# Kernel tuning notes

Hardware: AMD Instinct MI355X
Metric: run time of the kernel (lower is better)

## Reference

```python
import jax, jax.numpy as jnp
import numpy as np

SCALE = 8.0  # sqrt(d_head=64), per init_kwargs
B, H, S, D = 2, 16, 2048, 64


def setup_inputs() -> dict:
    key = jax.random.key(0)
    kq, kk, kv = jax.random.split(key, 3)
    q = jax.random.normal(kq, (B, H, S, D), dtype=jnp.float32)
    k = jax.random.normal(kk, (B, H, S, D), dtype=jnp.float32)
    v = jax.random.normal(kv, (B, H, S, D), dtype=jnp.float32)
    # causal mask: True where attention is NOT allowed (strictly upper triangle)
    causal = jnp.triu(jnp.ones((S, S), dtype=bool), k=1)
    mask = jnp.broadcast_to(causal, (B, H, S, S))
    return {"q": q, "k": k, "v": v, "mask": mask}


def reference(q, k, v, mask):
    # score = (q @ k^T) / scale, masked_fill(mask, -inf), softmax, @ v
    score = jnp.einsum('bhqd,bhkd->bhqk', q, k) / SCALE
    score = jnp.where(mask, -jnp.inf, score)
    attn = jax.nn.softmax(score, axis=-1)
    output = jnp.einsum('bhqk,bhkd->bhqd', attn, v)
    return (attn, output)
```

## Files before the change

kernel.cpp:

```cpp
#include <hip/hip_runtime.h>
#include <hip/hip_bf16.h>

#define S_LEN 2048
#define D_HEAD 64
#define SD (S_LEN * D_HEAD)
#define TILE_B 8192
#define NTILES 32

typedef __attribute__((ext_vector_type(8))) short short8;
typedef __attribute__((ext_vector_type(4))) float f32x4;

__device__ __forceinline__ unsigned short f2b(float f) {
  unsigned int u = __float_as_uint(f);
  u += 0x7fffu + ((u >> 16) & 1u);
  return (unsigned short)(u >> 16);
}

__device__ __forceinline__ float b2f(unsigned short s) {
  return __uint_as_float(((unsigned int)s) << 16);
}

__device__ __forceinline__ void gl_lds16(const void* g, void* l) {
  __builtin_amdgcn_global_load_lds(
      (const __attribute__((address_space(1))) unsigned int*)g,
      (__attribute__((address_space(3))) unsigned int*)l, 16, 0, 0);
}

__device__ __forceinline__ void stage8k(const char* gsrc, char* ldst, int w, int lane) {
  gl_lds16(gsrc + ((w * 64 + lane) << 4),        ldst + ((w * 64) << 4));
  gl_lds16(gsrc + ((256 + w * 64 + lane) << 4),  ldst + ((256 + w * 64) << 4));
}

__global__ __launch_bounds__(256) void convert_kv_kernel(
    const float* __restrict__ K, const float* __restrict__ V,
    char* __restrict__ Kpre, char* __restrict__ Vpre) {
  const int bid = blockIdx.x;
  const int tid = threadIdx.x;
  if (bid < 1024) {
    const int bh = bid >> 5, tile = bid & 31;
    const float* Kb = K + (size_t)bh * SD + tile * 64 * 64;
    char* out = Kpre + (size_t)bid * TILE_B;
    #pragma unroll
    for (int j = 0; j < 2; ++j) {
      int c = tid + j * 256;
      int sl = c >> 3;
      int d0 = ((c & 7) ^ (sl & 7)) << 3;
      const float* src = Kb + sl * 64 + d0;
      float4 a = *(const float4*)src;
      float4 b = *(const float4*)(src + 4);
      short8 o;
      o[0]=(short)f2b(a.x); o[1]=(short)f2b(a.y); o[2]=(short)f2b(a.z); o[3]=(short)f2b(a.w);
      o[4]=(short)f2b(b.x); o[5]=(short)f2b(b.y); o[6]=(short)f2b(b.z); o[7]=(short)f2b(b.w);
      *(short8*)(out + c * 16) = o;
    }
  } else {
    __shared__ float Vl[64][65];
    const int vb = bid - 1024;
    const int bh = vb >> 5, tile = vb & 31;
    const float* Vb = V + (size_t)bh * SD + tile * 64 * 64;
    #pragma unroll
    for (int j = 0; j < 4; ++j) {
      int row = (tid >> 4) + j * 16;
      int c4 = (tid & 15) << 2;
      float4 v = *(const float4*)(Vb + row * 64 + c4);
      Vl[row][c4+0] = v.x; Vl[row][c4+1] = v.y; Vl[row][c4+2] = v.z; Vl[row][c4+3] = v.w;
    }
    __syncthreads();
    char* out = Vpre + (size_t)vb * TILE_B;
    #pragma unroll
    for (int j = 0; j < 2; ++j) {
      int c = tid + j * 256;
      int d = c >> 3;
      int s0 = ((c & 7) ^ ((d >> 2) & 7)) << 3;
      short8 o;
      #pragma unroll
      for (int i = 0; i < 8; ++i) o[i] = (short)f2b(Vl[s0 + i][d]);
      *(short8*)(out + c * 16) = o;
    }
  }
}

__global__ __launch_bounds__(256, 4) void sdpa_pre_kernel(
    const float* __restrict__ Qg, const char* __restrict__ Kpre,
    const char* __restrict__ Vpre, float* __restrict__ attn,
    float* __restrict__ outp) {
  const int j  = blockIdx.x >> 8;
  const int rr = blockIdx.x & 255;
  const int xcd = rr & 7;
  const int cu  = rr >> 3;
  const int bh  = xcd + ((cu & 3) << 3);
  const int u   = cu >> 2;
  const int qt  = (j == 0) ? u : (j == 1) ? (15 - u) : (j == 2) ? (16 + u) : (31 - u);

  const int tid = threadIdx.x, wave = tid >> 6, lane = tid & 63;
  const int g = lane >> 4, m = lane & 15;
  const int swzK = (m & 7) << 4;

  __shared__ __align__(16) unsigned short Kl[2][4096];
  __shared__ __align__(16) unsigned short Vt[2][4096];
  __shared__ __align__(16) unsigned short Pl[4][1024];
  char* const PB = (char*)(&Pl[wave][0]);

  const size_t bhSD = (size_t)bh * SD;
  const size_t bhSS = (size_t)bh << 22;
  const char* KpreBH = Kpre + (size_t)bh * NTILES * TILE_B;
  const char* VpreBH = Vpre + (size_t)bh * NTILES * TILE_B;

  int vro[4], vsz[4];
  #pragma unroll
  for (int dc = 0; dc < 4; ++dc) {
    int d = dc * 16 + m;
    vro[dc] = d << 7;
    vsz[dc] = ((d >> 2) & 7) << 4;
  }
  const float SCL = 0.18033688011112042f;

  const int q0 = qt << 6;
  const int nIt = qt + 1;
  const int qwrow = q0 + wave * 16;
  const int qbase = qwrow + g * 4;

  short8 aq0, aq1;
  {
    const float* qp = Qg + bhSD + (size_t)(qwrow + m) * D_HEAD + g * 8;
    float4 x0 = *(const float4*)(qp);
    float4 x1 = *(const float4*)(qp + 4);
    float4 y0 = *(const float4*)(qp + 32);
    float4 y1 = *(const float4*)(qp + 36);
    aq0[0]=(short)f2b(x0.x*SCL); aq0[1]=(short)f2b(x0.y*SCL);
    aq0[2]=(short)f2b(x0.z*SCL); aq0[3]=(short)f2b(x0.w*SCL);
    aq0[4]=(short)f2b(x1.x*SCL); aq0[5]=(short)f2b(x1.y*SCL);
    aq0[6]=(short)f2b(x1.z*SCL); aq0[7]=(short)f2b(x1.w*SCL);
    aq1[0]=(short)f2b(y0.x*SCL); aq1[1]=(short)f2b(y0.y*SCL);
    aq1[2]=(short)f2b(y0.z*SCL); aq1[3]=(short)f2b(y0.w*SCL);
    aq1[4]=(short)f2b(y1.x*SCL); aq1[5]=(short)f2b(y1.y*SCL);
    aq1[6]=(short)f2b(y1.z*SCL); aq1[7]=(short)f2b(y1.w*SCL);
  }

  float rs0 = 0.f, rs1 = 0.f, rs2 = 0.f, rs3 = 0.f;
  __builtin_amdgcn_s_barrier();
  stage8k(KpreBH, (char*)Kl[0], wave, lane);
  int cur = 0;
  for (int it = 0; it < nIt; ++it) {
    asm volatile("s_waitcnt vmcnt(0)" ::: "memory");
    __builtin_amdgcn_s_barrier();
    __builtin_amdgcn_sched_barrier(0);
    if (it + 1 < nIt)
      stage8k(KpreBH + (size_t)(it + 1) * TILE_B, (char*)Kl[cur ^ 1], wave, lane);
    asm volatile("" ::: "memory");
    const char* KB = (const char*)Kl[cur];
    const int kc = it << 6;
    #pragma unroll
    for (int t = 0; t < 4; ++t) {
      f32x4 acc = {0.f, 0.f, 0.f, 0.f};
      const int rb = (t * 16 + m) << 7;
      short8 b0 = *(const short8*)(KB + ((rb + g * 16) ^ swzK));
      short8 b1 = *(const short8*)(KB + ((rb + 64 + g * 16) ^ swzK));
      acc = __builtin_amdgcn_mfma_f32_16x16x32_bf16(aq0, b0, acc, 0, 0, 0);
      acc = __builtin_amdgcn_mfma_f32_16x16x32_bf16(aq1, b1, acc, 0, 0, 0);
      const int kcol = kc + t * 16 + m;
      rs0 += (kcol <= qbase + 0) ? exp2f(acc[0]) : 0.f;
      rs1 += (kcol <= qbase + 1) ? exp2f(acc[1]) : 0.f;
      rs2 += (kcol <= qbase + 2) ? exp2f(acc[2]) : 0.f;
      rs3 += (kcol <= qbase + 3) ? exp2f(acc[3]) : 0.f;
    }
    cur ^= 1;
  }
  #pragma unroll
  for (int sft = 1; sft < 16; sft <<= 1) {
    rs0 += __shfl_xor(rs0, sft, 64);
    rs1 += __shfl_xor(rs1, sft, 64);
    rs2 += __shfl_xor(rs2, sft, 64);
    rs3 += __shfl_xor(rs3, sft, 64);
  }
  const float ri0 = 1.f / rs0, ri1 = 1.f / rs1, ri2 = 1.f / rs2, ri3 = 1.f / rs3;

  f32x4 o0 = {0.f,0.f,0.f,0.f}, o1 = {0.f,0.f,0.f,0.f};
  f32x4 o2 = {0.f,0.f,0.f,0.f}, o3 = {0.f,0.f,0.f,0.f};
  __builtin_amdgcn_s_barrier();
  stage8k(KpreBH, (char*)Kl[0], wave, lane);
  stage8k(VpreBH, (char*)Vt[0], wave, lane);
  cur = 0;
  const int sr = lane >> 2;
  const int cq = lane & 3;
  for (int it = 0; it < nIt; ++it) {
    if (it == 0) { asm volatile("s_waitcnt vmcnt(0)" ::: "memory"); }
    else         { asm volatile("s_waitcnt vmcnt(4)" ::: "memory"); }
    __builtin_amdgcn_s_barrier();
    __builtin_amdgcn_sched_barrier(0);
    if (it + 1 < nIt) {
      stage8k(KpreBH + (size_t)(it + 1) * TILE_B, (char*)Kl[cur ^ 1], wave, lane);
      stage8k(VpreBH + (size_t)(it + 1) * TILE_B, (char*)Vt[cur ^ 1], wave, lane);
    }
    asm volatile("" ::: "memory");
    const char* KB = (const char*)Kl[cur];
    const char* VB = (const char*)Vt[cur];
    const int kc = it << 6;
    #pragma unroll
    for (int t = 0; t < 4; ++t) {
      f32x4 acc = {0.f, 0.f, 0.f, 0.f};
      const int rb = (t * 16 + m) << 7;
      short8 b0 = *(const short8*)(KB + ((rb + g * 16) ^ swzK));
      short8 b1 = *(const short8*)(KB + ((rb + 64 + g * 16) ^ swzK));
      acc = __builtin_amdgcn_mfma_f32_16x16x32_bf16(aq0, b0, acc, 0, 0, 0);
      acc = __builtin_amdgcn_mfma_f32_16x16x32_bf16(aq1, b1, acc, 0, 0, 0);
      const int kcol = kc + t * 16 + m;
      const int tc = t * 16 + m;
      float p0 = (kcol <= qbase + 0) ? exp2f(acc[0]) * ri0 : 0.f;
      float p1 = (kcol <= qbase + 1) ? exp2f(acc[1]) * ri1 : 0.f;
      float p2 = (kcol <= qbase + 2) ? exp2f(acc[2]) * ri2 : 0.f;
      float p3 = (kcol <= qbase + 3) ? exp2f(acc[3]) * ri3 : 0.f;
      const int r0 = g * 4, c2 = tc << 1;
      *(unsigned short*)(PB + ((((r0+0)<<7) + c2) ^ (((r0+0)&7)<<4))) = f2b(p0);
      *(unsigned short*)(PB + ((((r0+1)<<7) + c2) ^ (((r0+1)&7)<<4))) = f2b(p1);
      *(unsigned short*)(PB + ((((r0+2)<<7) + c2) ^ (((r0+2)&7)<<4))) = f2b(p2);
      *(unsigned short*)(PB + ((((r0+3)<<7) + c2) ^ (((r0+3)&7)<<4))) = f2b(p3);
    }
    {
      float* arow = attn + bhSS + (size_t)(qwrow + sr) * S_LEN + kc + cq * 16;
      #pragma unroll
      for (int h = 0; h < 2; ++h) {
        const int off = (((sr << 7) + (cq << 5) + (h << 4))) ^ ((sr & 7) << 4);
        short8 pr = *(const short8*)(PB + off);
        float4 fa, fb;
        fa.x = b2f((unsigned short)pr[0]); fa.y = b2f((unsigned short)pr[1]);
        fa.z = b2f((unsigned short)pr[2]); fa.w = b2f((unsigned short)pr[3]);
        fb.x = b2f((unsigned short)pr[4]); fb.y = b2f((unsigned short)pr[5]);
        fb.z = b2f((unsigned short)pr[6]); fb.w = b2f((unsigned short)pr[7]);
        *(float4*)(arow + 8 * h)     = fa;
        *(float4*)(arow + 8 * h + 4) = fb;
      }
    }
    short8 pa0 = *(const short8*)(PB + (((m << 7) + g * 16) ^ swzK));
    short8 pa1 = *(const short8*)(PB + (((m << 7) + 64 + g * 16) ^ swzK));
    #pragma unroll
    for (int dc = 0; dc < 4; ++dc) {
      short8 bv0 = *(const short8*)(VB + ((vro[dc] + g * 16) ^ vsz[dc]));
      short8 bv1 = *(const short8*)(VB + ((vro[dc] + 64 + g * 16) ^ vsz[dc]));
      f32x4& od = (dc == 0) ? o0 : (dc == 1) ? o1 : (dc == 2) ? o2 : o3;
      od = __builtin_amdgcn_mfma_f32_16x16x32_bf16(pa0, bv0, od, 0, 0, 0);
      od = __builtin_amdgcn_mfma_f32_16x16x32_bf16(pa1, bv1, od, 0, 0, 0);
    }
    cur ^= 1;
  }

  #pragma unroll
  for (int reg = 0; reg < 4; ++reg) {
    float* op = outp + bhSD + (size_t)(qbase + reg) * D_HEAD + m;
    op[ 0] = o0[reg];
    op[16] = o1[reg];
    op[32] = o2[reg];
    op[48] = o3[reg];
  }

  const int col0 = nIt << 6;
  const int nvec = (S_LEN - col0) >> 2;
  if (nvec > 0) {
    const float4 z = {0.f, 0.f, 0.f, 0.f};
    for (int r = 0; r < 64; ++r) {
      float4* rp = (float4*)(attn + bhSS + (size_t)(q0 + r) * S_LEN + col0);
      for (int i = tid; i < nvec; i += 256) rp[i] = z;
    }
  }
}

__global__ __launch_bounds__(256) void sdpa_fb_kernel(
    const float* __restrict__ Qg, const float* __restrict__ Kg,
    const float* __restrict__ Vg, float* __restrict__ attn,
    float* __restrict__ outp) {
  const int bh = blockIdx.x >> 4;
  const int pi = blockIdx.x & 15;
  const int tid  = threadIdx.x;
  const int wave = tid >> 6;
  const int lane = tid & 63;
  const int g = lane >> 4;
  const int m = lane & 15;
  const int swzK = (m & 7) << 4;
  __shared__ __align__(16) unsigned short Kl[2][64 * 64];
  __shared__ __align__(16) unsigned short Vt[2][64 * 64];
  __shared__ __align__(16) unsigned short Pl[4][16 * 64];
  char* const PB = (char*)(&Pl[wave][0]);
  const size_t bhSD = (size_t)bh * (S_LEN * D_HEAD);
  const size_t bhSS = (size_t)bh * ((size_t)S_LEN * S_LEN);
  int ss[4], dd[4], koff[4];
  #pragma unroll
  for (int j = 0; j < 4; ++j) {
    int f = tid + j * 256;
    ss[j] = f >> 4;
    dd[j] = (f & 15) << 2;
    koff[j] = (((ss[j] << 6) + dd[j]) << 1) ^ ((ss[j] & 7) << 4);
  }
  int vro[4], vsz[4];
  #pragma unroll
  for (int dc = 0; dc < 4; ++dc) {
    int d = dc * 16 + m;
    vro[dc] = d << 7;
    vsz[dc] = ((d >> 2) & 7) << 4;
  }
  const float SCL = 0.18033688011112042f;
  for (int sidx = 0; sidx < 2; ++sidx) {
    const int qt = sidx ? (31 - pi) : pi;
    const int q0 = qt << 6;
    const int kmax = q0 + 64;
    const int nIter = kmax >> 6;
    const int qwrow = q0 + wave * 16;
    const int qbase = qwrow + g * 4;
    short8 aq0, aq1;
    {
      const float* qp = Qg + bhSD + (size_t)(qwrow + m) * D_HEAD + g * 8;
      float4 x0 = *(const float4*)(qp);
      float4 x1 = *(const float4*)(qp + 4);
      float4 y0 = *(const float4*)(qp + 32);
      float4 y1 = *(const float4*)(qp + 36);
      aq0[0]=(short)f2b(x0.x*SCL); aq0[1]=(short)f2b(x0.y*SCL);
      aq0[2]=(short)f2b(x0.z*SCL); aq0[3]=(short)f2b(x0.w*SCL);
      aq0[4]=(short)f2b(x1.x*SCL); aq0[5]=(short)f2b(x1.y*SCL);
      aq0[6]=(short)f2b(x1.z*SCL); aq0[7]=(short)f2b(x1.w*SCL);
      aq1[0]=(short)f2b(y0.x*SCL); aq1[1]=(short)f2b(y0.y*SCL);
      aq1[2]=(short)f2b(y0.z*SCL); aq1[3]=(short)f2b(y0.w*SCL);
      aq1[4]=(short)f2b(y1.x*SCL); aq1[5]=(short)f2b(y1.y*SCL);
      aq1[6]=(short)f2b(y1.z*SCL); aq1[7]=(short)f2b(y1.w*SCL);
    }
    float rs0 = 0.f, rs1 = 0.f, rs2 = 0.f, rs3 = 0.f;
    {
      float4 kr[4];
      #pragma unroll
      for (int j = 0; j < 4; ++j)
        kr[j] = *(const float4*)(Kg + bhSD + (size_t)ss[j] * D_HEAD + dd[j]);
      #pragma unroll
      for (int j = 0; j < 4; ++j) {
        ushort4 kb;
        kb.x = f2b(kr[j].x); kb.y = f2b(kr[j].y);
        kb.z = f2b(kr[j].z); kb.w = f2b(kr[j].w);
        *(ushort4*)((char*)Kl[0] + koff[j]) = kb;
      }
    }
    __syncthreads();
    int cur = 0;
    for (int it = 0; it < nIter; ++it) {
      const int kc = it << 6;
      const bool pf = (it + 1 < nIter);
      float4 kr[4];
      if (pf) {
        #pragma unroll
        for (int j = 0; j < 4; ++j)
          kr[j] = *(const float4*)(Kg + bhSD + (size_t)(kc + 64 + ss[j]) * D_HEAD + dd[j]);
      }
      const char* KB = (const char*)Kl[cur];
      #pragma unroll
      for (int t = 0; t < 4; ++t) {
        f32x4 acc = {0.f, 0.f, 0.f, 0.f};
        const int rb = (t * 16 + m) << 7;
        short8 b0 = *(const short8*)(KB + ((rb + g * 16) ^ swzK));
        short8 b1 = *(const short8*)(KB + ((rb + 64 + g * 16) ^ swzK));
        acc = __builtin_amdgcn_mfma_f32_16x16x32_bf16(aq0, b0, acc, 0, 0, 0);
        acc = __builtin_amdgcn_mfma_f32_16x16x32_bf16(aq1, b1, acc, 0, 0, 0);
        const int kcol = kc + t * 16 + m;
        rs0 += (kcol <= qbase + 0) ? exp2f(acc[0]) : 0.f;
        rs1 += (kcol <= qbase + 1) ? exp2f(acc[1]) : 0.f;
        rs2 += (kcol <= qbase + 2) ? exp2f(acc[2]) : 0.f;
        rs3 += (kcol <= qbase + 3) ? exp2f(acc[3]) : 0.f;
      }
      if (pf) {
        #pragma unroll
        for (int j = 0; j < 4; ++j) {
          ushort4 kb;
          kb.x = f2b(kr[j].x); kb.y = f2b(kr[j].y);
          kb.z = f2b(kr[j].z); kb.w = f2b(kr[j].w);
          *(ushort4*)((char*)Kl[cur ^ 1] + koff[j]) = kb;
        }
      }
      __syncthreads();
      cur ^= 1;
    }
    #pragma unroll
    for (int sft = 1; sft < 16; sft <<= 1) {
      rs0 += __shfl_xor(rs0, sft, 64);
      rs1 += __shfl_xor(rs1, sft, 64);
      rs2 += __shfl_xor(rs2, sft, 64);
      rs3 += __shfl_xor(rs3, sft, 64);
    }
    const float ri0 = 1.f / rs0, ri1 = 1.f / rs1, ri2 = 1.f / rs2, ri3 = 1.f / rs3;
    f32x4 o0 = {0.f,0.f,0.f,0.f}, o1 = {0.f,0.f,0.f,0.f};
    f32x4 o2 = {0.f,0.f,0.f,0.f}, o3 = {0.f,0.f,0.f,0.f};
    {
      float4 kr[4], vr[4];
      #pragma unroll
      for (int j = 0; j < 4; ++j) {
        kr[j] = *(const float4*)(Kg + bhSD + (size_t)ss[j] * D_HEAD + dd[j]);
        vr[j] = *(const float4*)(Vg + bhSD + (size_t)ss[j] * D_HEAD + dd[j]);
      }
      #pragma unroll
      for (int j = 0; j < 4; ++j) {
        ushort4 kb;
        kb.x = f2b(kr[j].x); kb.y = f2b(kr[j].y);
        kb.z = f2b(kr[j].z); kb.w = f2b(kr[j].w);
        *(ushort4*)((char*)Kl[0] + koff[j]) = kb;
        const int d0 = dd[j], s2 = ss[j] << 1;
        char* VB1 = (char*)Vt[0];
        *(unsigned short*)(VB1 + ((((d0+0)<<7) + s2) ^ ((((d0+0)>>2)&7)<<4))) = f2b(vr[j].x);
        *(unsigned short*)(VB1 + ((((d0+1)<<7) + s2) ^ ((((d0+1)>>2)&7)<<4))) = f2b(vr[j].y);
        *(unsigned short*)(VB1 + ((((d0+2)<<7) + s2) ^ ((((d0+2)>>2)&7)<<4))) = f2b(vr[j].z);
        *(unsigned short*)(VB1 + ((((d0+3)<<7) + s2) ^ ((((d0+3)>>2)&7)<<4))) = f2b(vr[j].w);
      }
    }
    __syncthreads();
    cur = 0;
    for (int it = 0; it < nIter; ++it) {
      const int kc = it << 6;
      const bool pf = (it + 1 < nIter);
      float4 kr[4], vr[4];
      if (pf) {
        #pragma unroll
        for (int j = 0; j < 4; ++j) {
          kr[j] = *(const float4*)(Kg + bhSD + (size_t)(kc + 64 + ss[j]) * D_HEAD + dd[j]);
          vr[j] = *(const float4*)(Vg + bhSD + (size_t)(kc + 64 + ss[j]) * D_HEAD + dd[j]);
        }
      }
      const char* KB = (const char*)Kl[cur];
      const char* VB = (const char*)Vt[cur];
      float* arow = attn + bhSS + (size_t)qbase * S_LEN + kc;
      #pragma unroll
      for (int t = 0; t < 4; ++t) {
        f32x4 acc = {0.f, 0.f, 0.f, 0.f};
        const int rb = (t * 16 + m) << 7;
        short8 b0 = *(const short8*)(KB + ((rb + g * 16) ^ swzK));
        short8 b1 = *(const short8*)(KB + ((rb + 64 + g * 16) ^ swzK));
        acc = __builtin_amdgcn_mfma_f32_16x16x32_bf16(aq0, b0, acc, 0, 0, 0);
        acc = __builtin_amdgcn_mfma_f32_16x16x32_bf16(aq1, b1, acc, 0, 0, 0);
        const int kcol = kc + t * 16 + m;
        const int tc = t * 16 + m;
        float p0 = (kcol <= qbase + 0) ? exp2f(acc[0]) * ri0 : 0.f;
        float p1 = (kcol <= qbase + 1) ? exp2f(acc[1]) * ri1 : 0.f;
        float p2 = (kcol <= qbase + 2) ? exp2f(acc[2]) * ri2 : 0.f;
        float p3 = (kcol <= qbase + 3) ? exp2f(acc[3]) * ri3 : 0.f;
        arow[0 * S_LEN + tc] = p0;
        arow[1 * S_LEN + tc] = p1;
        arow[2 * S_LEN + tc] = p2;
        arow[3 * S_LEN + tc] = p3;
        const int r0 = g * 4, c2 = tc << 1;
        *(unsigned short*)(PB + ((((r0+0)<<7) + c2) ^ (((r0+0)&7)<<4))) = f2b(p0);
        *(unsigned short*)(PB + ((((r0+1)<<7) + c2) ^ (((r0+1)&7)<<4))) = f2b(p1);
        *(unsigned short*)(PB + ((((r0+2)<<7) + c2) ^ (((r0+2)&7)<<4))) = f2b(p2);
        *(unsigned short*)(PB + ((((r0+3)<<7) + c2) ^ (((r0+3)&7)<<4))) = f2b(p3);
      }
      short8 pa0 = *(const short8*)(PB + (((m << 7) + g * 16) ^ swzK));
      short8 pa1 = *(const short8*)(PB + (((m << 7) + 64 + g * 16) ^ swzK));
      #pragma unroll
      for (int dc = 0; dc < 4; ++dc) {
        short8 bv0 = *(const short8*)(VB + ((vro[dc] + g * 16) ^ vsz[dc]));
        short8 bv1 = *(const short8*)(VB + ((vro[dc] + 64 + g * 16) ^ vsz[dc]));
        f32x4& od = (dc == 0) ? o0 : (dc == 1) ? o1 : (dc == 2) ? o2 : o3;
        od = __builtin_amdgcn_mfma_f32_16x16x32_bf16(pa0, bv0, od, 0, 0, 0);
        od = __builtin_amdgcn_mfma_f32_16x16x32_bf16(pa1, bv1, od, 0, 0, 0);
      }
      if (pf) {
        #pragma unroll
        for (int j = 0; j < 4; ++j) {
          ushort4 kb;
          kb.x = f2b(kr[j].x); kb.y = f2b(kr[j].y);
          kb.z = f2b(kr[j].z); kb.w = f2b(kr[j].w);
          *(ushort4*)((char*)Kl[cur ^ 1] + koff[j]) = kb;
          const int d0 = dd[j], s2 = ss[j] << 1;
          char* VB1 = (char*)Vt[cur ^ 1];
          *(unsigned short*)(VB1 + ((((d0+0)<<7) + s2) ^ ((((d0+0)>>2)&7)<<4))) = f2b(vr[j].x);
          *(unsigned short*)(VB1 + ((((d0+1)<<7) + s2) ^ ((((d0+1)>>2)&7)<<4))) = f2b(vr[j].y);
          *(unsigned short*)(VB1 + ((((d0+2)<<7) + s2) ^ ((((d0+2)>>2)&7)<<4))) = f2b(vr[j].z);
          *(unsigned short*)(VB1 + ((((d0+3)<<7) + s2) ^ ((((d0+3)>>2)&7)<<4))) = f2b(vr[j].w);
        }
      }
      __syncthreads();
      cur ^= 1;
    }
    #pragma unroll
    for (int reg = 0; reg < 4; ++reg) {
      float* op = outp + bhSD + (size_t)(qbase + reg) * D_HEAD + m;
      op[ 0] = o0[reg];
      op[16] = o1[reg];
      op[32] = o2[reg];
      op[48] = o3[reg];
    }
    const int ncols = S_LEN - kmax;
    if (ncols > 0) {
      const float4 z = {0.f, 0.f, 0.f, 0.f};
      const int nvec = ncols >> 2;
      for (int r = 0; r < 64; ++r) {
        float4* rp = (float4*)(attn + bhSS + (size_t)(q0 + r) * S_LEN + kmax);
        for (int i = tid; i < nvec; i += 256) rp[i] = z;
      }
    }
  }
}

extern "C" void kernel_launch(void* const* d_in, const int* in_sizes, int n_in,
                              void* d_out, int out_size, void* d_ws, size_t ws_size,
                              hipStream_t stream) {
  (void)in_sizes; (void)n_in; (void)out_size;
  const float* q = (const float*)d_in[0];
  const float* k = (const float*)d_in[1];
  const float* v = (const float*)d_in[2];
  float* attn = (float*)d_out;
  float* outp = attn + (size_t)2 * 16 * 2048 * 2048;
  const size_t pre_bytes = (size_t)32 * NTILES * TILE_B;
  if (ws_size >= 2 * pre_bytes) {
    char* Kpre = (char*)d_ws;
    char* Vpre = Kpre + pre_bytes;
    convert_kv_kernel<<<2048, 256, 0, stream>>>(k, v, Kpre, Vpre);
    sdpa_pre_kernel<<<1024, 256, 0, stream>>>(q, Kpre, Vpre, attn, outp);
  } else {
    sdpa_fb_kernel<<<512, 256, 0, stream>>>(q, k, v, attn, outp);
  }
}
```

Baseline: 179.8 us.

## Interleave attention zero-fill into first pass and specialize unmasked tiles

Moves the zero-filling of the masked upper-triangle attn region out of the kernel tail and spreads it across the iterations of the first (row-sum) pass. The global stores can then overlap with the MFMA and exp work instead of running as a serial epilogue. It also splits both passes into a fast path for tiles fully below the diagonal, which skips the per-element causal compare, and keeps the masked path for diagonal tiles. The cost is larger code and added integer division work in the fill loop. The fill's stores may also compete with the K staging loads.

```diff
diff --git a/kernel.cpp b/kernel.cpp
--- a/kernel.cpp
+++ b/kernel.cpp
@@ -137,6 +137,14 @@
     aq1[6]=(short)f2b(y1.z*SCL); aq1[7]=(short)f2b(y1.w*SCL);
   }
 
+  const int ncols = S_LEN - (nIt << 6);
+  const int nvpr = ncols >> 2;
+  const int T = ncols >> 4;
+  const int F = (T + nIt - 1) / nIt;
+  int vb = 0;
+  float* const fillb = attn + bhSS + (size_t)q0 * S_LEN + (nIt << 6);
+  const float4 z4 = {0.f, 0.f, 0.f, 0.f};
+
   float rs0 = 0.f, rs1 = 0.f, rs2 = 0.f, rs3 = 0.f;
   __builtin_amdgcn_s_barrier();
   stage8k(KpreBH, (char*)Kl[0], wave, lane);
@@ -147,22 +155,47 @@
     __builtin_amdgcn_sched_barrier(0);
     if (it + 1 < nIt)
       stage8k(KpreBH + (size_t)(it + 1) * TILE_B, (char*)Kl[cur ^ 1], wave, lane);
+    if (T > 0) {
+      int ve = vb + F; if (ve > T) ve = T;
+      for (; vb < ve; ++vb) {
+        int gv = vb * 256 + tid;
+        int row = (unsigned)gv / (unsigned)nvpr;
+        int cv = gv - row * nvpr;
+        *(float4*)(fillb + (size_t)row * S_LEN + (cv << 2)) = z4;
+      }
+    }
     asm volatile("" ::: "memory");
     const char* KB = (const char*)Kl[cur];
     const int kc = it << 6;
-    #pragma unroll
-    for (int t = 0; t < 4; ++t) {
-      f32x4 acc = {0.f, 0.f, 0.f, 0.f};
-      const int rb = (t * 16 + m) << 7;
-      short8 b0 = *(const short8*)(KB + ((rb + g * 16) ^ swzK));
-      short8 b1 = *(const short8*)(KB + ((rb + 64 + g * 16) ^ swzK));
-      acc = __builtin_amdgcn_mfma_f32_16x16x32_bf16(aq0, b0, acc, 0, 0, 0);
-      acc = __builtin_amdgcn_mfma_f32_16x16x32_bf16(aq1, b1, acc, 0, 0, 0);
-      const int kcol = kc + t * 16 + m;
-      rs0 += (kcol <= qbase + 0) ? exp2f(acc[0]) : 0.f;
-      rs1 += (kcol <= qbase + 1) ? exp2f(acc[1]) : 0.f;
-      rs2 += (kcol <= qbase + 2) ? exp2f(acc[2]) : 0.f;
-      rs3 += (kcol <= qbase + 3) ? exp2f(acc[3]) : 0.f;
+    if (kc + 64 <= qwrow) {
+      #pragma unroll
+      for (int t = 0; t < 4; ++t) {
+        f32x4 acc = {0.f, 0.f, 0.f, 0.f};
+        const int rb = (t * 16 + m) << 7;
+        short8 b0 = *(const short8*)(KB + ((rb + g * 16) ^ swzK));
+        short8 b1 = *(const short8*)(KB + ((rb + 64 + g * 16) ^ swzK));
+        acc = __builtin_amdgcn_mfma_f32_16x16x32_bf16(aq0, b0, acc, 0, 0, 0);
+        acc = __builtin_amdgcn_mfma_f32_16x16x32_bf16(aq1, b1, acc, 0, 0, 0);
+        rs0 += exp2f(acc[0]);
+        rs1 += exp2f(acc[1]);
+        rs2 += exp2f(acc[2]);
+        rs3 += exp2f(acc[3]);
+      }
+    } else {
+      #pragma unroll
+      for (int t = 0; t < 4; ++t) {
+        f32x4 acc = {0.f, 0.f, 0.f, 0.f};
+        const int rb = (t * 16 + m) << 7;
+        short8 b0 = *(const short8*)(KB + ((rb + g * 16) ^ swzK));
+        short8 b1 = *(const short8*)(KB + ((rb + 64 + g * 16) ^ swzK));
+        acc = __builtin_amdgcn_mfma_f32_16x16x32_bf16(aq0, b0, acc, 0, 0, 0);
+        acc = __builtin_amdgcn_mfma_f32_16x16x32_bf16(aq1, b1, acc, 0, 0, 0);
+        const int kcol = kc + t * 16 + m;
+        rs0 += (kcol <= qbase + 0) ? exp2f(acc[0]) : 0.f;
+        rs1 += (kcol <= qbase + 1) ? exp2f(acc[1]) : 0.f;
+        rs2 += (kcol <= qbase + 2) ? exp2f(acc[2]) : 0.f;
+        rs3 += (kcol <= qbase + 3) ? exp2f(acc[3]) : 0.f;
+      }
     }
     cur ^= 1;
   }
@@ -196,25 +229,47 @@
     const char* KB = (const char*)Kl[cur];
     const char* VB = (const char*)Vt[cur];
     const int kc = it << 6;
-    #pragma unroll
-    for (int t = 0; t < 4; ++t) {
-      f32x4 acc = {0.f, 0.f, 0.f, 0.f};
-      const int rb = (t * 16 + m) << 7;
-      short8 b0 = *(const short8*)(KB + ((rb + g * 16) ^ swzK));
-      short8 b1 = *(const short8*)(KB + ((rb + 64 + g * 16) ^ swzK));
-      acc = __builtin_amdgcn_mfma_f32_16x16x32_bf16(aq0, b0, acc, 0, 0, 0);
-      acc = __builtin_amdgcn_mfma_f32_16x16x32_bf16(aq1, b1, acc, 0, 0, 0);
-      const int kcol = kc + t * 16 + m;
-      const int tc = t * 16 + m;
-      float p0 = (kcol <= qbase + 0) ? exp2f(acc[0]) * ri0 : 0.f;
-      float p1 = (kcol <= qbase + 1) ? exp2f(acc[1]) * ri1 : 0.f;
-      float p2 = (kcol <= qbase + 2) ? exp2f(acc[2]) * ri2 : 0.f;
-      float p3 = (kcol <= qbase + 3) ? exp2f(acc[3]) * ri3 : 0.f;
-      const int r0 = g * 4, c2 = tc << 1;
-      *(unsigned short*)(PB + ((((r0+0)<<7) + c2) ^ (((r0+0)&7)<<4))) = f2b(p0);
-      *(unsigned short*)(PB + ((((r0+1)<<7) + c2) ^ (((r0+1)&7)<<4))) = f2b(p1);
-      *(unsigned short*)(PB + ((((r0+2)<<7) + c2) ^ (((r0+2)&7)<<4))) = f2b(p2);
-      *(unsigned short*)(PB + ((((r0+3)<<7) + c2) ^ (((r0+3)&7)<<4))) = f2b(p3);
+    if (kc + 64 <= qwrow) {
+      #pragma unroll
+      for (int t = 0; t < 4; ++t) {
+        f32x4 acc = {0.f, 0.f, 0.f, 0.f};
+        const int rb = (t * 16 + m) << 7;
+        short8 b0 = *(const short8*)(KB + ((rb + g * 16) ^ swzK));
+        short8 b1 = *(const short8*)(KB + ((rb + 64 + g * 16) ^ swzK));
+        acc = __builtin_amdgcn_mfma_f32_16x16x32_bf16(aq0, b0, acc, 0, 0, 0);
+        acc = __builtin_amdgcn_mfma_f32_16x16x32_bf16(aq1, b1, acc, 0, 0, 0);
+        const int tc = t * 16 + m;
+        float p0 = exp2f(acc[0]) * ri0;
+        float p1 = exp2f(acc[1]) * ri1;
+        float p2 = exp2f(acc[2]) * ri2;
+        float p3 = exp2f(acc[3]) * ri3;
+        const int r0 = g * 4, c2 = tc << 1;
+        *(unsigned short*)(PB + ((((r0+0)<<7) + c2) ^ (((r0+0)&7)<<4))) = f2b(p0);
+        *(unsigned short*)(PB + ((((r0+1)<<7) + c2) ^ (((r0+1)&7)<<4))) = f2b(p1);
+        *(unsigned short*)(PB + ((((r0+2)<<7) + c2) ^ (((r0+2)&7)<<4))) = f2b(p2);
+        *(unsigned short*)(PB + ((((r0+3)<<7) + c2) ^ (((r0+3)&7)<<4))) = f2b(p3);
+      }
+    } else {
+      #pragma unroll
+      for (int t = 0; t < 4; ++t) {
+        f32x4 acc = {0.f, 0.f, 0.f, 0.f};
+        const int rb = (t * 16 + m) << 7;
+        short8 b0 = *(const short8*)(KB + ((rb + g * 16) ^ swzK));
+        short8 b1 = *(const short8*)(KB + ((rb + 64 + g * 16) ^ swzK));
+        acc = __builtin_amdgcn_mfma_f32_16x16x32_bf16(aq0, b0, acc, 0, 0, 0);
+        acc = __builtin_amdgcn_mfma_f32_16x16x32_bf16(aq1, b1, acc, 0, 0, 0);
+        const int kcol = kc + t * 16 + m;
+        const int tc = t * 16 + m;
+        float p0 = (kcol <= qbase + 0) ? exp2f(acc[0]) * ri0 : 0.f;
+        float p1 = (kcol <= qbase + 1) ? exp2f(acc[1]) * ri1 : 0.f;
+        float p2 = (kcol <= qbase + 2) ? exp2f(acc[2]) * ri2 : 0.f;
+        float p3 = (kcol <= qbase + 3) ? exp2f(acc[3]) * ri3 : 0.f;
+        const int r0 = g * 4, c2 = tc << 1;
+        *(unsigned short*)(PB + ((((r0+0)<<7) + c2) ^ (((r0+0)&7)<<4))) = f2b(p0);
+        *(unsigned short*)(PB + ((((r0+1)<<7) + c2) ^ (((r0+1)&7)<<4))) = f2b(p1);
+        *(unsigned short*)(PB + ((((r0+2)<<7) + c2) ^ (((r0+2)&7)<<4))) = f2b(p2);
+        *(unsigned short*)(PB + ((((r0+3)<<7) + c2) ^ (((r0+3)&7)<<4))) = f2b(p3);
+      }
     }
     {
       float* arow = attn + bhSS + (size_t)(qwrow + sr) * S_LEN + kc + cq * 16;
@@ -251,16 +306,6 @@
     op[16] = o1[reg];
     op[32] = o2[reg];
     op[48] = o3[reg];
-  }
-
-  const int col0 = nIt << 6;
-  const int nvec = (S_LEN - col0) >> 2;
-  if (nvec > 0) {
-    const float4 z = {0.f, 0.f, 0.f, 0.f};
-    for (int r = 0; r < 64; ++r) {
-      float4* rp = (float4*)(attn + bhSS + (size_t)(q0 + r) * S_LEN + col0);
-      for (int i = tid; i < nvec; i += 256) rp[i] = z;
-    }
   }
 }
 
```

Result: slower. 206.9 us (+15.0%).
